# Optimization experiments

Measured on AMD Instinct MI355X. Metric: run time of the kernel, lower is better.

## Reference

```python
import jax, jax.numpy as jnp
import numpy as np

K_NN = 3  # pointnet2 relation default k=3


def setup_inputs() -> dict:
    key = jax.random.key(0)
    k1, k2, k3 = jax.random.split(key, 3)
    B, N, S, C = 4, 16384, 4096, 256
    q = jax.random.normal(k1, (B, N, 3), dtype=jnp.float32)
    k = jax.random.normal(k2, (B, S, 3), dtype=jnp.float32)
    v = jax.random.normal(k3, (B, S, C), dtype=jnp.float32)
    return {"q": q, "k": k, "v": v}


def reference(q, k, v):
    # squared pairwise distance: ||q||^2 - 2 q.k + ||k||^2  -> [B, N, S]
    d = (
        jnp.sum(q * q, axis=-1, keepdims=True)
        - 2.0 * jnp.einsum("bnd,bsd->bns", q, k)
        + jnp.sum(k * k, axis=-1)[:, None, :]
    )
    # 3 nearest neighbors (smallest distances)
    neg_d, idx = jax.lax.top_k(-d, K_NN)          # [B, N, 3]
    dists = -neg_d
    recip = 1.0 / (dists + 1e-8)
    weight = recip / jnp.sum(recip, axis=-1, keepdims=True)  # [B, N, 3]
    # score is zero except at idx; scatter+dense matmul == gather-weighted sum
    B = q.shape[0]
    vg = v[jnp.arange(B)[:, None, None], idx]     # [B, N, 3, C]
    extract = jnp.einsum("bnk,bnkc->bnc", weight, vg)  # [B, N, C]
    return jnp.transpose(extract, (0, 2, 1))      # [B, C, N] (embed is identity)
```

## Files before the change

kernel.cpp:

```cpp
#include <hip/hip_runtime.h>

#define BB 4
#define NN 16384
#define SS 4096
#define CC 256
#define SEG 1024
#define RQ 4
#define TILE_LD 260

__device__ __forceinline__ bool lexlt(float da, int ia, float db, int ib) {
  return (da < db) || ((da == db) && (ia < ib));
}

__global__ __launch_bounds__(256, 8) void scan_kernel(
    const float* __restrict__ qg, const float* __restrict__ kg,
    float4* __restrict__ dpart, int4* __restrict__ ipart) {
#pragma clang fp contract(off)
  __shared__ __align__(16) float4 kpts[SEG];
  float* md = (float*)kpts;
  int* mi = (int*)((char*)kpts + 6144);

  const int tid = threadIdx.x;
  const int blk = blockIdx.x;
  const int b = blk >> 9;
  const int seg = (blk >> 7) & 3;
  const int n0 = (blk & 127) << 7;
  const int qlane = tid & 31;
  const int g = tid >> 5;

  float qx[RQ], qy[RQ], qz[RQ], qq[RQ];
  float d0[RQ], d1[RQ], d2[RQ];
  int i0[RQ], i1[RQ], i2[RQ];
#pragma unroll
  for (int j = 0; j < RQ; ++j) {
    int n = n0 + qlane + 32 * j;
    const float* qp = qg + ((long)b * NN + n) * 3;
    qx[j] = qp[0]; qy[j] = qp[1]; qz[j] = qp[2];
    qq[j] = (qx[j] * qx[j] + qy[j] * qy[j]) + qz[j] * qz[j];
    d0[j] = 3.4e38f; d1[j] = 3.4e38f; d2[j] = 3.4e38f;
    i0[j] = 0; i1[j] = 0; i2[j] = 0;
  }

  {
    const float* kb = kg + ((long)b * SS + (long)seg * SEG) * 3;
    const float4* src = (const float4*)kb + tid * 3;
    float4 f0 = src[0], f1 = src[1], f2 = src[2];
    float px[4] = {f0.x, f0.w, f1.z, f2.y};
    float py[4] = {f0.y, f1.x, f1.w, f2.z};
    float pz[4] = {f0.z, f1.y, f2.x, f2.w};
#pragma unroll
    for (int m = 0; m < 4; ++m) {
      float kk = (px[m] * px[m] + py[m] * py[m]) + pz[m] * pz[m];
      kpts[tid * 4 + m] = make_float4(px[m], py[m], pz[m], kk);
    }
  }
  __syncthreads();

  const int sbase = seg * SEG + g * 128;
#pragma unroll 2
  for (int i = 0; i < 128; ++i) {
    float4 kp = kpts[g * 128 + i];
    const int s = sbase + i;
#pragma unroll
    for (int j = 0; j < RQ; ++j) {
      float dot = (qx[j] * kp.x + qy[j] * kp.y) + qz[j] * kp.z;
      float d = __builtin_fmaf(dot, -2.0f, qq[j]) + kp.w;
      bool k2 = d < d2[j];
      bool k1 = d < d1[j];
      bool k0 = d < d0[j];
      float nd2 = __builtin_amdgcn_fmed3f(d, d1[j], d2[j]);
      float nd1 = __builtin_amdgcn_fmed3f(d, d0[j], d1[j]);
      float nd0 = fminf(d, d0[j]);
      i2[j] = k1 ? i1[j] : (k2 ? s : i2[j]);
      i1[j] = k0 ? i0[j] : (k1 ? s : i1[j]);
      i0[j] = k0 ? s : i0[j];
      d2[j] = nd2; d1[j] = nd1; d0[j] = nd0;
    }
  }

#pragma unroll
  for (int j = 0; j < RQ; ++j) {
    float E0 = __shfl_xor(d0[j], 32), E1 = __shfl_xor(d1[j], 32), E2 = __shfl_xor(d2[j], 32);
    int F0 = __shfl_xor(i0[j], 32), F1 = __shfl_xor(i1[j], 32), F2 = __shfl_xor(i2[j], 32);
    float A0 = d0[j], A1 = d1[j], A2 = d2[j];
    int B0 = i0[j], B1 = i1[j], B2 = i2[j];
    bool t = lexlt(E0, F0, A0, B0);
    float r0 = t ? E0 : A0; int s0 = t ? F0 : B0;
    float nA0 = t ? A0 : A1, nA1 = t ? A1 : A2;
    int nB0 = t ? B0 : B1, nB1 = t ? B1 : B2;
    float nE0 = t ? E1 : E0, nE1 = t ? E2 : E1;
    int nF0 = t ? F1 : F0, nF1 = t ? F2 : F1;
    bool u = lexlt(nE0, nF0, nA0, nB0);
    float r1 = u ? nE0 : nA0; int s1 = u ? nF0 : nB0;
    float mA0 = u ? nA0 : nA1; int mB0 = u ? nB0 : nB1;
    float mE0 = u ? nE1 : nE0; int mF0 = u ? nF1 : nF0;
    bool w = lexlt(mE0, mF0, mA0, mB0);
    float r2 = w ? mE0 : mA0; int s2 = w ? mF0 : mB0;
    d0[j] = r0; d1[j] = r1; d2[j] = r2;
    i0[j] = s0; i1[j] = s1; i2[j] = s2;
  }

  __syncthreads();
  if ((tid & 63) < 32) {
    const int wv = tid >> 6;
#pragma unroll
    for (int j = 0; j < RQ; ++j) {
      int base = (((wv * 32) + qlane) * RQ + j) * 3;
      md[base + 0] = d0[j]; md[base + 1] = d1[j]; md[base + 2] = d2[j];
      mi[base + 0] = i0[j]; mi[base + 1] = i1[j]; mi[base + 2] = i2[j];
    }
  }
  __syncthreads();

  if (tid < 128) {
    const int qi = tid;
    const int ql = qi & 31, jj = qi >> 5;
    float D0 = 3.4e38f, D1 = 3.4e38f, D2 = 3.4e38f;
    int I0 = -1, I1 = -1, I2 = -1;
    for (int wv = 0; wv < 4; ++wv) {
      int base = ((wv * 32 + ql) * RQ + jj) * 3;
      for (int r = 0; r < 3; ++r) {
        float d = md[base + r];
        int s = mi[base + r];
        if (lexlt(d, s, D2, I2)) {
          if (lexlt(d, s, D1, I1)) {
            D2 = D1; I2 = I1;
            if (lexlt(d, s, D0, I0)) { D1 = D0; I1 = I0; D0 = d; I0 = s; }
            else { D1 = d; I1 = s; }
          } else { D2 = d; I2 = s; }
        }
      }
    }
    long gid = (long)b * NN + n0 + qi;
    dpart[gid * 4 + seg] = make_float4(D0, D1, D2, 0.0f);
    ipart[gid * 4 + seg] = make_int4(I0, I1, I2, 0);
  }
}

__global__ __launch_bounds__(256, 4) void gather_kernel(
    const float* __restrict__ vg, const float4* __restrict__ dpart,
    const int4* __restrict__ ipart, float* __restrict__ outg) {
#pragma clang fp contract(off)
  __shared__ __align__(16) float tile[32 * TILE_LD];
  __shared__ float sw[32][3];
  __shared__ int si[32][3];

  const int tid = threadIdx.x;
  const int blk = blockIdx.x;
  const int b = blk >> 9;
  const int n0 = (blk & 511) << 5;

  if (tid < 32) {
    long gid = (long)b * NN + n0 + tid;
    float D0 = 3.4e38f, D1 = 3.4e38f, D2 = 3.4e38f;
    int I0 = -1, I1 = -1, I2 = -1;
#pragma unroll
    for (int seg = 0; seg < 4; ++seg) {
      float4 dv = dpart[gid * 4 + seg];
      int4 iv = ipart[gid * 4 + seg];
      float ds_[3] = {dv.x, dv.y, dv.z};
      int is_[3] = {iv.x, iv.y, iv.z};
      for (int r = 0; r < 3; ++r) {
        float d = ds_[r];
        int s = is_[r];
        if (lexlt(d, s, D2, I2)) {
          if (lexlt(d, s, D1, I1)) {
            D2 = D1; I2 = I1;
            if (lexlt(d, s, D0, I0)) { D1 = D0; I1 = I0; D0 = d; I0 = s; }
            else { D1 = d; I1 = s; }
          } else { D2 = d; I2 = s; }
        }
      }
    }
    float r0 = 1.0f / (D0 + 1e-8f);
    float r1 = 1.0f / (D1 + 1e-8f);
    float r2 = 1.0f / (D2 + 1e-8f);
    float rs = (r0 + r1) + r2;
    sw[tid][0] = r0 / rs; sw[tid][1] = r1 / rs; sw[tid][2] = r2 / rs;
    si[tid][0] = I0; si[tid][1] = I1; si[tid][2] = I2;
  }
  __syncthreads();

  const int wv = tid >> 6;
  const int lane = tid & 63;
  const float* vb = vg + (long)b * SS * CC;

#pragma unroll 2
  for (int i = 0; i < 8; ++i) {
    int qs = wv * 8 + i;
    float w0 = sw[qs][0], w1 = sw[qs][1], w2 = sw[qs][2];
    const float4* r0p = (const float4*)(vb + (long)si[qs][0] * CC);
    const float4* r1p = (const float4*)(vb + (long)si[qs][1] * CC);
    const float4* r2p = (const float4*)(vb + (long)si[qs][2] * CC);
    float4 a0 = r0p[lane], a1 = r1p[lane], a2 = r2p[lane];
    float4 acc;
    acc.x = (w0 * a0.x + w1 * a1.x) + w2 * a2.x;
    acc.y = (w0 * a0.y + w1 * a1.y) + w2 * a2.y;
    acc.z = (w0 * a0.z + w1 * a1.z) + w2 * a2.z;
    acc.w = (w0 * a0.w + w1 * a1.w) + w2 * a2.w;
    *(float4*)&tile[qs * TILE_LD + lane * 4] = acc;
  }
  __syncthreads();
  {
    int qs2 = tid & 31;
    int cb = tid >> 5;
    long nout = (long)n0 + qs2;
    for (int it = 0; it < 32; ++it) {
      int cch = cb + it * 8;
      outg[((long)(b * CC + cch)) * NN + nout] = tile[qs2 * TILE_LD + cch];
    }
  }
}

extern "C" void kernel_launch(void* const* d_in, const int* in_sizes, int n_in,
                              void* d_out, int out_size, void* d_ws, size_t ws_size,
                              hipStream_t stream) {
  const float* q = (const float*)d_in[0];
  const float* k = (const float*)d_in[1];
  const float* v = (const float*)d_in[2];
  float* out = (float*)d_out;
  float4* dpart = (float4*)d_ws;
  int4* ipart = (int4*)((char*)d_ws + (size_t)BB * NN * 4 * 16);
  hipLaunchKernelGGL(scan_kernel, dim3(2048), dim3(256), 0, stream, q, k, dpart, ipart);
  hipLaunchKernelGGL(gather_kernel, dim3(2048), dim3(256), 0, stream, v, dpart, ipart, out);
}
```

Measured before the change: 231.9 us.

## Split gather transpose into channel halves with float4 output stores

The gather kernel now handles the 256 channels in two 128-channel chunks. This halves the shared-memory transpose tile, so launch bounds can request 8 blocks per CU instead of 4. The transposed write-out now has each thread store a float4 covering 4 consecutive query points rather than scalar stores, which cuts the number of global store instructions. In exchange it adds an extra barrier per chunk, and the strided LDS reads during the transpose may cause bank conflicts.

```diff
diff --git a/kernel.cpp b/kernel.cpp
--- a/kernel.cpp
+++ b/kernel.cpp
@@ -6,7 +6,7 @@
 #define CC 256
 #define SEG 1024
 #define RQ 4
-#define TILE_LD 260
+#define TLD 132
 
 __device__ __forceinline__ bool lexlt(float da, int ia, float db, int ib) {
   return (da < db) || ((da == db) && (ia < ib));
@@ -137,11 +137,11 @@
   }
 }
 
-__global__ __launch_bounds__(256, 4) void gather_kernel(
+__global__ __launch_bounds__(256, 8) void gather_kernel(
     const float* __restrict__ vg, const float4* __restrict__ dpart,
     const int4* __restrict__ ipart, float* __restrict__ outg) {
 #pragma clang fp contract(off)
-  __shared__ __align__(16) float tile[32 * TILE_LD];
+  __shared__ __align__(16) float tile[32 * TLD];
   __shared__ float sw[32][3];
   __shared__ int si[32][3];
 
@@ -183,32 +183,45 @@
 
   const int wv = tid >> 6;
   const int lane = tid & 63;
+  const int qh = lane >> 5;
+  const int slot = lane & 31;
   const float* vb = vg + (long)b * SS * CC;
 
+  const int nf = tid & 7;
+  const int cb0 = tid >> 3;
+
+#pragma unroll
+  for (int chunk = 0; chunk < 2; ++chunk) {
+    const int coff = chunk << 5;
 #pragma unroll 2
-  for (int i = 0; i < 8; ++i) {
-    int qs = wv * 8 + i;
-    float w0 = sw[qs][0], w1 = sw[qs][1], w2 = sw[qs][2];
-    const float4* r0p = (const float4*)(vb + (long)si[qs][0] * CC);
-    const float4* r1p = (const float4*)(vb + (long)si[qs][1] * CC);
-    const float4* r2p = (const float4*)(vb + (long)si[qs][2] * CC);
-    float4 a0 = r0p[lane], a1 = r1p[lane], a2 = r2p[lane];
-    float4 acc;
-    acc.x = (w0 * a0.x + w1 * a1.x) + w2 * a2.x;
-    acc.y = (w0 * a0.y + w1 * a1.y) + w2 * a2.y;
-    acc.z = (w0 * a0.z + w1 * a1.z) + w2 * a2.z;
-    acc.w = (w0 * a0.w + w1 * a1.w) + w2 * a2.w;
-    *(float4*)&tile[qs * TILE_LD + lane * 4] = acc;
-  }
-  __syncthreads();
-  {
-    int qs2 = tid & 31;
-    int cb = tid >> 5;
-    long nout = (long)n0 + qs2;
-    for (int it = 0; it < 32; ++it) {
-      int cch = cb + it * 8;
-      outg[((long)(b * CC + cch)) * NN + nout] = tile[qs2 * TILE_LD + cch];
-    }
+    for (int it = 0; it < 4; ++it) {
+      int qs = wv * 8 + it * 2 + qh;
+      float w0 = sw[qs][0], w1 = sw[qs][1], w2 = sw[qs][2];
+      const float4* r0p = (const float4*)(vb + (long)si[qs][0] * CC) + coff;
+      const float4* r1p = (const float4*)(vb + (long)si[qs][1] * CC) + coff;
+      const float4* r2p = (const float4*)(vb + (long)si[qs][2] * CC) + coff;
+      float4 a0 = r0p[slot], a1 = r1p[slot], a2 = r2p[slot];
+      float4 acc;
+      acc.x = (w0 * a0.x + w1 * a1.x) + w2 * a2.x;
+      acc.y = (w0 * a0.y + w1 * a1.y) + w2 * a2.y;
+      acc.z = (w0 * a0.z + w1 * a1.z) + w2 * a2.z;
+      acc.w = (w0 * a0.w + w1 * a1.w) + w2 * a2.w;
+      *(float4*)&tile[qs * TLD + slot * 4] = acc;
+    }
+    __syncthreads();
+#pragma unroll 2
+    for (int it = 0; it < 4; ++it) {
+      int cl = cb0 + it * 32;
+      int cch = (chunk << 7) + cl;
+      int q0 = nf * 4;
+      float4 val;
+      val.x = tile[(q0 + 0) * TLD + cl];
+      val.y = tile[(q0 + 1) * TLD + cl];
+      val.z = tile[(q0 + 2) * TLD + cl];
+      val.w = tile[(q0 + 3) * TLD + cl];
+      *(float4*)&outg[((long)(b * CC + cch)) * NN + n0 + q0] = val;
+    }
+    __syncthreads();
   }
 }
 
```

Result: slower. 238.0 us (+2.6%).

## Remap gather blocks per XCD by batch/channel half and vectorize output stores

Applied to the files above, without the earlier changes.

The gather kernel now gives each block 64 queries by 128 channels. Block IDs are mapped so that each XCD serves one batch and one channel half, which shrinks the set of value rows each XCD's L2 must hold. The transposed output is written as 16-byte nontemporal stores of four consecutive queries instead of scalar stores. In exchange, the top-3 merge and weight computation run twice per query (once per channel half), and the stores depend on the assumed round-robin placement of blocks across XCDs.

```diff
diff --git a/kernel.cpp b/kernel.cpp
--- a/kernel.cpp
+++ b/kernel.cpp
@@ -6,7 +6,9 @@
 #define CC 256
 #define SEG 1024
 #define RQ 4
-#define TILE_LD 260
+#define TLD 132
+
+typedef float f32x4 __attribute__((ext_vector_type(4)));
 
 __device__ __forceinline__ bool lexlt(float da, int ia, float db, int ib) {
   return (da < db) || ((da == db) && (ia < ib));
@@ -141,16 +143,19 @@
     const float* __restrict__ vg, const float4* __restrict__ dpart,
     const int4* __restrict__ ipart, float* __restrict__ outg) {
 #pragma clang fp contract(off)
-  __shared__ __align__(16) float tile[32 * TILE_LD];
-  __shared__ float sw[32][3];
-  __shared__ int si[32][3];
+  __shared__ __align__(16) float tile[64 * TLD];
+  __shared__ float sw[64][3];
+  __shared__ int si[64][3];
 
   const int tid = threadIdx.x;
-  const int blk = blockIdx.x;
-  const int b = blk >> 9;
-  const int n0 = (blk & 511) << 5;
-
-  if (tid < 32) {
+  const int bid = blockIdx.x;
+  const int xcd = bid & 7;
+  const int b = xcd >> 1;
+  const int chunk = xcd & 1;
+  const int nblk = bid >> 3;
+  const int n0 = nblk << 6;
+
+  if (tid < 64) {
     long gid = (long)b * NN + n0 + tid;
     float D0 = 3.4e38f, D1 = 3.4e38f, D2 = 3.4e38f;
     int I0 = -1, I1 = -1, I2 = -1;
@@ -183,31 +188,42 @@
 
   const int wv = tid >> 6;
   const int lane = tid & 63;
-  const float* vb = vg + (long)b * SS * CC;
-
-#pragma unroll 2
-  for (int i = 0; i < 8; ++i) {
-    int qs = wv * 8 + i;
+  const int qh = lane >> 5;
+  const int slot = lane & 31;
+  const float* vb = vg + (long)b * SS * CC + chunk * 128;
+
+#pragma unroll 4
+  for (int it = 0; it < 8; ++it) {
+    int qs = wv * 16 + it * 2 + qh;
     float w0 = sw[qs][0], w1 = sw[qs][1], w2 = sw[qs][2];
     const float4* r0p = (const float4*)(vb + (long)si[qs][0] * CC);
     const float4* r1p = (const float4*)(vb + (long)si[qs][1] * CC);
     const float4* r2p = (const float4*)(vb + (long)si[qs][2] * CC);
-    float4 a0 = r0p[lane], a1 = r1p[lane], a2 = r2p[lane];
+    float4 a0 = r0p[slot], a1 = r1p[slot], a2 = r2p[slot];
     float4 acc;
     acc.x = (w0 * a0.x + w1 * a1.x) + w2 * a2.x;
     acc.y = (w0 * a0.y + w1 * a1.y) + w2 * a2.y;
     acc.z = (w0 * a0.z + w1 * a1.z) + w2 * a2.z;
     acc.w = (w0 * a0.w + w1 * a1.w) + w2 * a2.w;
-    *(float4*)&tile[qs * TILE_LD + lane * 4] = acc;
-  }
-  __syncthreads();
+    *(float4*)&tile[qs * TLD + slot * 4] = acc;
+  }
+  __syncthreads();
+
   {
-    int qs2 = tid & 31;
-    int cb = tid >> 5;
-    long nout = (long)n0 + qs2;
-    for (int it = 0; it < 32; ++it) {
-      int cch = cb + it * 8;
-      outg[((long)(b * CC + cch)) * NN + nout] = tile[qs2 * TILE_LD + cch];
+    const int nf = tid & 15;
+    const int cb0 = tid >> 4;
+    const int q0 = nf << 2;
+#pragma unroll 2
+    for (int it = 0; it < 8; ++it) {
+      int cl = cb0 + it * 16;
+      int cch = (chunk << 7) + cl;
+      f32x4 val;
+      val.x = tile[(q0 + 0) * TLD + cl];
+      val.y = tile[(q0 + 1) * TLD + cl];
+      val.z = tile[(q0 + 2) * TLD + cl];
+      val.w = tile[(q0 + 3) * TLD + cl];
+      __builtin_nontemporal_store(
+          val, (f32x4*)&outg[((long)(b * CC + cch)) * NN + n0 + q0]);
     }
   }
 }
```

Measured after the change: 227.1 us. 2.1% less time.
